# Optimization experiments

Hardware: AMD Instinct MI355X
Metric: run time of the kernel (lower is better)

Reference implementation:

```python
import jax, jax.numpy as jnp
import numpy as np

N, T = 4096, 1024
COND, PRED, PERIOD = 896, 56, 7


def setup_inputs() -> dict:
    key = jax.random.key(0)
    k1, k2 = jax.random.split(key)
    query = jax.random.normal(k1, (N, T), dtype=jnp.float32)
    # learned per-location params: [init_level, level_sm_logit, init_trend,
    #  trend_sm_logit, season_sm, period seasonality logits]
    params = 0.1 * jax.random.normal(k2, (N, 5 + PERIOD), dtype=jnp.float32)
    return {"query": query, "params": params}


def _forward(query, params):
    init_level = params[:, 0]                       # [N]
    level_sm = jax.nn.sigmoid(params[:, 1])         # [N]
    init_trend = params[:, 2]                       # [N]
    trend_sm = jax.nn.sigmoid(params[:, 3])         # [N]
    season_sm = params[:, 4]                        # NOTE: no sigmoid, matches original code
    init_seas = jax.nn.sigmoid(params[:, -PERIOD:])  # [N, PERIOD]

    def step(carry, y):
        prev_level, prev_trend, buf = carry          # buf: rolling window of last PERIOD seasonalities
        s_t = buf[:, 0]                              # seasonalities[t]
        pred = prev_level + prev_trend
        level = level_sm * y + (1.0 - level_sm) * pred
        diff = jnp.abs(level - prev_level)
        trend = trend_sm * (level - prev_level) + (1.0 - trend_sm) * prev_trend
        new_seas = season_sm * (y - pred) + (1.0 - season_sm) * s_t
        buf = jnp.concatenate([buf[:, 1:], new_seas[:, None]], axis=1)
        return (level, trend, buf), (level, trend, new_seas, diff)

    carry0 = (init_level, init_trend, init_seas)
    _, (levels, trends, new_seas_seq, diffs) = jax.lax.scan(step, carry0, query.T)
    levels = levels.T            # [N, T]
    trends = trends.T            # [N, T]
    new_seas_seq = new_seas_seq.T  # [N, T], == seasonalities[:, PERIOD:]
    level_diffs = diffs.T.mean(axis=1)  # [N]

    # full seasonality sequence: PERIOD initial values followed by T computed ones
    seas_full = jnp.concatenate([init_seas, new_seas_seq], axis=1)  # [N, PERIOD+T]

    sm = query - levels - new_seas_seq  # [N, T]

    horizon = jnp.arange(1, PRED + 1, dtype=levels.dtype)  # [PRED]
    last_levels = levels[:, COND - 1:, None]   # [N, W, 1], W = T-COND+1
    last_trends = trends[:, COND - 1:, None]
    pr = last_levels + last_trends * horizon   # [N, W, PRED]

    # cyclic seasonality forecast per window
    season_index = jnp.tile(jnp.arange(PERIOD), (PRED + PERIOD - 1) // PERIOD)[:PRED]
    starts = jnp.arange(COND, T + 1)           # [W]
    idx = starts[:, None] + season_index[None, :]  # [W, PRED]
    pr = pr + seas_full[:, idx]                # [N, W, PRED]

    return sm, pr, level_diffs


def reference(query, params):
    return _forward(query, params)
```

## Files before the change

kernel.cpp:

```cpp
#include <hip/hip_runtime.h>
#include <cmath>

#define NROWS 4096
#define TLEN  1024
#define RPB   8
#define LT0   895
#define ST0   889
#define LTN   129
#define STN   135
#define PRV4R 1806
#define PRV4B (RPB * PRV4R)

__device__ __forceinline__ float sigmoidf_(float x) {
    return 1.0f / (1.0f + expf(-x));
}

__device__ __forceinline__ float f4c(const float4& v, int k) {
    switch (k & 3) { case 0: return v.x; case 1: return v.y; case 2: return v.z; default: return v.w; }
}

__global__ __launch_bounds__(256, 2)
void es_fused(const float* __restrict__ query,
              const float* __restrict__ params,
              float* __restrict__ sm,
              float* __restrict__ diffs,
              float4* __restrict__ pr4)
{
    __shared__ float lds_P[RPB * 65];
    __shared__ float lds_start[RPB * 65];
    __shared__ float lds_q[RPB * 225];
    __shared__ float lds_dsum[RPB * 33];
    __shared__ float lds_par[RPB * 16];
    __shared__ float Ltl[RPB * 132];
    __shared__ float Ttl[RPB * 132];
    __shared__ float Stl[RPB * 136];

    const int tid = threadIdx.x;
    const int r = tid >> 5;
    const int k = tid & 31;
    const int n = blockIdx.x * RPB + r;

    const float* pp = params + (size_t)n * 12;
    const float a  = sigmoidf_(pp[1]);
    const float b  = sigmoidf_(pp[3]);
    const float c  = pp[4];
    const float ia = 1.0f - a, ib = 1.0f - b, ic = 1.0f - c;

    float4 yv[8];
    {
        const float4* qv = reinterpret_cast<const float4*>(query + (size_t)n * TLEN + k * 32);
        #pragma unroll
        for (int i = 0; i < 8; ++i) yv[i] = qv[i];
    }

    {
        float L = 0.0f, B = 0.0f;
        #pragma unroll
        for (int j = 0; j < 32; ++j) {
            const float yy = f4c(yv[j >> 2], j);
            const float pred  = L + B;
            const float level = fmaf(a, yy, ia * pred);
            const float trend = fmaf(b, level - L, ib * B);
            L = level; B = trend;
        }
        lds_P[r * 65 + 2 * k]     = L;
        lds_P[r * 65 + 2 * k + 1] = B;
    }
    if (k == 0) {
        float* par = &lds_par[r * 16];
        par[0] = pp[0];
        par[1] = pp[2];
        par[2] = ia;
        par[3] = -(a * b);
        par[4] = ib + b * ia;
        par[5] = ic;
        #pragma unroll
        for (int l = 0; l < 7; ++l) par[6 + l] = sigmoidf_(pp[5 + l]);
    }
    __syncthreads();

    if (tid < 8) {
        const float* par = &lds_par[tid * 16];
        float m00 = par[2], m01 = par[2], m10 = par[3], m11 = par[4];
        #pragma unroll
        for (int s = 0; s < 5; ++s) {
            const float t00 = m00 * m00 + m01 * m10;
            const float t01 = m00 * m01 + m01 * m11;
            const float t10 = m10 * m00 + m11 * m10;
            const float t11 = m10 * m01 + m11 * m11;
            m00 = t00; m01 = t01; m10 = t10; m11 = t11;
        }
        float P0[32], P1[32];
        #pragma unroll
        for (int kk = 0; kk < 32; ++kk) {
            P0[kk] = lds_P[tid * 65 + 2 * kk];
            P1[kk] = lds_P[tid * 65 + 2 * kk + 1];
        }
        float s0 = par[0], s1 = par[1];
        #pragma unroll
        for (int kk = 0; kk < 32; ++kk) {
            lds_start[tid * 65 + 2 * kk]     = s0;
            lds_start[tid * 65 + 2 * kk + 1] = s1;
            const float t0 = m00 * s0 + m01 * s1 + P0[kk];
            const float t1 = m10 * s0 + m11 * s1 + P1[kk];
            s0 = t0; s1 = t1;
        }
    }
    __syncthreads();

    const float st0 = lds_start[r * 65 + 2 * k];
    const float st1 = lds_start[r * 65 + 2 * k + 1];

    float e[32];
    {
        float L = st0, B = st1, dsum = 0.0f;
        float q[7] = {0,0,0,0,0,0,0};
        #pragma unroll
        for (int j = 0; j < 32; ++j) {
            const float yy = f4c(yv[j >> 2], j);
            const float pred  = L + B;
            const float level = fmaf(a, yy, ia * pred);
            const float d     = level - L;
            dsum += fabsf(d);
            const float trend = fmaf(b, d, ib * B);
            const float ee    = yy - pred;
            e[j] = ee;
            q[j % 7] = fmaf(ic, q[j % 7], c * ee);
            L = level; B = trend;
        }
        const int kp = (4 * k) % 7;
        #pragma unroll
        for (int l = 0; l < 7; ++l) {
            int g = kp + l; if (g >= 7) g -= 7;
            lds_q[r * 225 + k * 7 + g] = q[l];
        }
        lds_dsum[r * 33 + k] = dsum;
    }

    if (k >= 27) {
        float prevL = st0, Bv = st1;
        #pragma unroll
        for (int j = 0; j < 32; ++j) {
            const float level = f4c(yv[j >> 2], j) - ia * e[j];
            const float trend = fmaf(b, level - prevL, ib * Bv);
            const int tg = k * 32 + j;
            if (tg >= LT0) {
                Ltl[r * 132 + tg - LT0] = level;
                Ttl[r * 132 + tg - LT0] = trend;
            }
            prevL = level; Bv = trend;
        }
    }
    __syncthreads();

    if (tid < 56) {
        const int rr = tid / 7, p = tid % 7;
        const float icc = lds_par[rr * 16 + 5];
        const float ic2 = icc * icc;
        const float ic4 = ic2 * ic2;
        const float ic5 = ic4 * icc;
        float v = lds_par[rr * 16 + 6 + p];
        float qq[32];
        #pragma unroll
        for (int kk = 0; kk < 32; ++kk) qq[kk] = lds_q[rr * 225 + kk * 7 + p];
        int l = p;
        #pragma unroll
        for (int kk = 0; kk < 32; ++kk) {
            const float m = (l < 4) ? ic5 : ic4;
            const float nv = fmaf(m, v, qq[kk]);
            lds_q[rr * 225 + kk * 7 + p] = v;
            v = nv;
            l += 3; if (l >= 7) l -= 7;
        }
    } else if (tid < 64) {
        const int rr = tid - 56;
        float s = 0.0f;
        #pragma unroll
        for (int kk = 0; kk < 32; ++kk) s += lds_dsum[rr * 33 + kk];
        diffs[blockIdx.x * RPB + rr] = s * (1.0f / 1024.0f);
    }
    __syncthreads();

    {
        float sg[7];
        const int kp = (4 * k) % 7;
        #pragma unroll
        for (int l = 0; l < 7; ++l) {
            int g = kp + l; if (g >= 7) g -= 7;
            sg[l] = lds_q[r * 225 + k * 7 + g];
        }
        float4 ov;
        float* smrow = sm + (size_t)n * TLEN + k * 32;
        #pragma unroll
        for (int j = 0; j < 32; ++j) {
            const float sn = fmaf(ic, sg[j % 7], c * e[j]);
            sg[j % 7] = sn;
            const float smv = ia * e[j] - sn;
            switch (j & 3) { case 0: ov.x = smv; break; case 1: ov.y = smv; break;
                             case 2: ov.z = smv; break; default: ov.w = smv; }
            if ((j & 3) == 3) *reinterpret_cast<float4*>(smrow + (j - 3)) = ov;
            const int tg = k * 32 + j;
            if (tg >= ST0) Stl[r * 136 + tg - ST0] = sn;
        }
    }
    __syncthreads();

    {
        float4* prb = pr4 + (size_t)blockIdx.x * PRV4B;
        #pragma unroll 4
        for (int i = 0; i < 57; ++i) {
            const int q = i * 256 + tid;
            if (q < PRV4B) {
                const int row = q / PRV4R;
                const int rem = q - row * PRV4R;
                const int s   = rem / 14;
                const int h4  = rem - s * 14;
                const float L = Ltl[row * 132 + s];
                const float T = Ttl[row * 132 + s];
                const float* stp = &Stl[row * 136 + s];
                const int hb = h4 * 4;
                int m0 = hb % 7;
                int m1 = m0 + 1; if (m1 >= 7) m1 -= 7;
                int m2 = m0 + 2; if (m2 >= 7) m2 -= 7;
                int m3 = m0 + 3; if (m3 >= 7) m3 -= 7;
                float4 o;
                o.x = fmaf(T, (float)(hb + 1), L) + stp[m0];
                o.y = fmaf(T, (float)(hb + 2), L) + stp[m1];
                o.z = fmaf(T, (float)(hb + 3), L) + stp[m2];
                o.w = fmaf(T, (float)(hb + 4), L) + stp[m3];
                prb[q] = o;
            }
        }
    }
}

extern "C" void kernel_launch(void* const* d_in, const int* in_sizes, int n_in,
                              void* d_out, int out_size, void* d_ws, size_t ws_size,
                              hipStream_t stream) {
    const float* query  = (const float*)d_in[0];
    const float* params = (const float*)d_in[1];

    float* out   = (float*)d_out;
    float* sm    = out;
    float* pr    = out + (size_t)NROWS * TLEN;
    float* diffs = pr  + (size_t)NROWS * 129 * 56;

    hipLaunchKernelGGL(es_fused, dim3(NROWS / RPB), dim3(256), 0, stream,
                       query, params, sm, diffs, (float4*)pr);
}
```

Measured before the change: 37.34 us.

## Stage query loads and sm stores through swizzled LDS for coalesced global access

```diff
diff --git a/kernel.cpp b/kernel.cpp
--- a/kernel.cpp
+++ b/kernel.cpp
@@ -26,6 +26,7 @@
               float* __restrict__ diffs,
               float4* __restrict__ pr4)
 {
+    __shared__ float4 ystage[RPB * 256];
     __shared__ float lds_P[RPB * 65];
     __shared__ float lds_start[RPB * 65];
     __shared__ float lds_q[RPB * 225];
@@ -38,7 +39,16 @@
     const int tid = threadIdx.x;
     const int r = tid >> 5;
     const int k = tid & 31;
-    const int n = blockIdx.x * RPB + r;
+    const int base = blockIdx.x * RPB;
+    const int n = base + r;
+
+    {
+        const float4* qb = reinterpret_cast<const float4*>(query + (size_t)base * TLEN);
+        const int cs = tid ^ ((tid >> 3) & 7);
+        #pragma unroll
+        for (int i = 0; i < 8; ++i)
+            ystage[i * 256 + cs] = qb[i * 256 + tid];
+    }
 
     const float* pp = params + (size_t)n * 12;
     const float a  = sigmoidf_(pp[1]);
@@ -46,11 +56,14 @@
     const float c  = pp[4];
     const float ia = 1.0f - a, ib = 1.0f - b, ic = 1.0f - c;
 
+    __syncthreads();
+
     float4 yv[8];
     {
-        const float4* qv = reinterpret_cast<const float4*>(query + (size_t)n * TLEN + k * 32);
-        #pragma unroll
-        for (int i = 0; i < 8; ++i) yv[i] = qv[i];
+        const int ksw = k & 7;
+        #pragma unroll
+        for (int i = 0; i < 8; ++i)
+            yv[i] = ystage[r * 256 + ((k * 8 + i) ^ ksw)];
     }
 
     {
@@ -189,47 +202,64 @@
             int g = kp + l; if (g >= 7) g -= 7;
             sg[l] = lds_q[r * 225 + k * 7 + g];
         }
+        const int ksw = k & 7;
         float4 ov;
-        float* smrow = sm + (size_t)n * TLEN + k * 32;
         #pragma unroll
         for (int j = 0; j < 32; ++j) {
             const float sn = fmaf(ic, sg[j % 7], c * e[j]);
             sg[j % 7] = sn;
             const float smv = ia * e[j] - sn;
+            e[j] = sn;
             switch (j & 3) { case 0: ov.x = smv; break; case 1: ov.y = smv; break;
                              case 2: ov.z = smv; break; default: ov.w = smv; }
-            if ((j & 3) == 3) *reinterpret_cast<float4*>(smrow + (j - 3)) = ov;
-            const int tg = k * 32 + j;
-            if (tg >= ST0) Stl[r * 136 + tg - ST0] = sn;
-        }
-    }
-    __syncthreads();
+            if ((j & 3) == 3)
+                ystage[r * 256 + ((k * 8 + (j >> 2)) ^ ksw)] = ov;
+        }
+        if (k >= 27) {
+            #pragma unroll
+            for (int j = 0; j < 32; ++j) {
+                const int tg = k * 32 + j;
+                if (tg >= ST0) Stl[r * 136 + tg - ST0] = e[j];
+            }
+        }
+    }
+    __syncthreads();
+
+    {
+        float4* smb = reinterpret_cast<float4*>(sm + (size_t)base * TLEN);
+        const int cs = tid ^ ((tid >> 3) & 7);
+        #pragma unroll
+        for (int i = 0; i < 8; ++i)
+            smb[i * 256 + tid] = ystage[i * 256 + cs];
+    }
 
     {
         float4* prb = pr4 + (size_t)blockIdx.x * PRV4B;
-        #pragma unroll 4
+        int row = 0;
+        int s   = tid / 14;
+        int h4  = tid - s * 14;
+        int m0  = (4 * h4) % 7;
         for (int i = 0; i < 57; ++i) {
             const int q = i * 256 + tid;
             if (q < PRV4B) {
-                const int row = q / PRV4R;
-                const int rem = q - row * PRV4R;
-                const int s   = rem / 14;
-                const int h4  = rem - s * 14;
                 const float L = Ltl[row * 132 + s];
                 const float T = Ttl[row * 132 + s];
                 const float* stp = &Stl[row * 136 + s];
-                const int hb = h4 * 4;
-                int m0 = hb % 7;
                 int m1 = m0 + 1; if (m1 >= 7) m1 -= 7;
-                int m2 = m0 + 2; if (m2 >= 7) m2 -= 7;
-                int m3 = m0 + 3; if (m3 >= 7) m3 -= 7;
+                int m2 = m1 + 1; if (m2 >= 7) m2 -= 7;
+                int m3 = m2 + 1; if (m3 >= 7) m3 -= 7;
+                const float hb = (float)(h4 * 4);
                 float4 o;
-                o.x = fmaf(T, (float)(hb + 1), L) + stp[m0];
-                o.y = fmaf(T, (float)(hb + 2), L) + stp[m1];
-                o.z = fmaf(T, (float)(hb + 3), L) + stp[m2];
-                o.w = fmaf(T, (float)(hb + 4), L) + stp[m3];
+                o.x = fmaf(T, hb + 1.0f, L) + stp[m0];
+                o.y = fmaf(T, hb + 2.0f, L) + stp[m1];
+                o.z = fmaf(T, hb + 3.0f, L) + stp[m2];
+                o.w = fmaf(T, hb + 4.0f, L) + stp[m3];
                 prb[q] = o;
             }
+            h4 += 4; s += 18;
+            if (h4 >= 14) { h4 -= 14; s += 1; }
+            if (s >= 129) { s -= 129; row += 1; }
+            m0 += 2; if (m0 >= 7) m0 -= 7;
         }
     }
 }
```

New measurement: 35.74 us. 1.04x faster.
